# Optimization experiments

Measured on AMD Instinct MI355X. Metric: run time of the kernel, lower is better.

## Reference

```python
import jax, jax.numpy as jnp
import numpy as np
from jax import lax

B, F, N = 1024, 512, 8  # batch, feature_dim, num_of_subAttention


def setup_inputs() -> dict:
    key = jax.random.key(0)
    ks = jax.random.split(key, 8)
    sc = 0.02
    return {
        "vx": jax.random.normal(ks[0], (B, F), dtype=jnp.float32),
        "ax": jax.random.normal(ks[1], (B, F), dtype=jnp.float32),
        # stacked per-unit MLP params (N units)
        "W1": jax.random.normal(ks[2], (N, F, 2 * F), dtype=jnp.float32) * sc,
        "b1": jnp.zeros((N, F), jnp.float32),
        "W2": jax.random.normal(ks[3], (N, F, F), dtype=jnp.float32) * sc,
        "b2": jnp.zeros((N, F), jnp.float32),
        # conv pipeline params (OIHW)
        "conv1_w": jax.random.normal(ks[4], (F, F, 3, 3), dtype=jnp.float32) * sc,
        "conv1_b": jnp.zeros((F,), jnp.float32),
        "conv2_w": jax.random.normal(ks[5], (F, F, 3, 3), dtype=jnp.float32) * sc,
        "conv2_b": jnp.zeros((F,), jnp.float32),
    }


def reference(vx, ax, W1, b1, W2, b2, conv1_w, conv1_b, conv2_w, conv2_b):
    # --- N AttentionUnits, vectorized over the unit axis n ---
    x = jnp.concatenate([vx, ax], axis=-1)                      # [B, 2F]
    # Dropout(0.5) is identity in eval mode.
    h = jax.nn.relu(jnp.einsum('bi,nfi->bnf', x, W1) + b1)      # [B, N, F]
    att = jax.nn.relu(jnp.einsum('bnf,ngf->bng', h, W2) + b2)   # [B, N, F]

    # vx broadcast over units, elementwise attention, then permute to [B, F, N]
    va = jnp.transpose(vx[:, None, :] * att, (0, 2, 1))         # [B, F, N]
    # rank-1 broadcast along trailing axis -> conv input [B, F, N, N]
    t = jnp.broadcast_to(va[..., None], (B, F, N, N))

    dn = ('NCHW', 'OIHW', 'NCHW')
    y = lax.conv_general_dilated(t, conv1_w, (1, 1), 'SAME', dimension_numbers=dn)
    y = y + conv1_b[None, :, None, None]
    k = N // 2
    y = lax.reduce_window(y, -jnp.inf, lax.max, (1, 1, k, k), (1, 1, k, k), 'VALID')  # [B,F,2,2]
    y = lax.conv_general_dilated(y, conv2_w, (1, 1), 'SAME', dimension_numbers=dn)
    y = y + conv2_b[None, :, None, None]
    y = jnp.mean(y, axis=(2, 3))                                # AdaptiveAvgPool2d((1,1)) -> [B, F]
    return jax.nn.relu(y)
```

## Files before the change

kernel.cpp:

```cpp
#include <hip/hip_runtime.h>
#include <hip/hip_bf16.h>


typedef __attribute__((ext_vector_type(8))) short short8;
typedef __attribute__((ext_vector_type(4))) float f32x4;

__device__ __forceinline__ void gload16(const void* g, void* l) {
    __builtin_amdgcn_global_load_lds(
        (const __attribute__((address_space(1))) void*)g,
        (__attribute__((address_space(3))) void*)l, 16, 0, 0);
}

template<int BM, int BN, bool RELU, bool BIAS, bool OUT_BF16, bool SWAP>
__global__ __launch_bounds__(256) void gemm_mfma(
    const __hip_bfloat16* __restrict__ A, int lda, long sA,
    const __hip_bfloat16* __restrict__ B, int ldb, long sB,
    void* __restrict__ Cv, int ldc, long sC,
    const float* __restrict__ bias, long sBias,
    int K)
{
    constexpr int MI = BM / 32, NI = BN / 32;
    constexpr int GA = BM / 16, GB = BN / 16;
    constexpr int nA = (GA * 2) / 4, nB = (GB * 2) / 4;
    __shared__ __align__(16) char As[128 * BM];
    __shared__ __align__(16) char Bs[128 * BN];

    const int z = blockIdx.z;
    A += (long)z * sA;
    B += (long)z * sB;
    const int bm = (SWAP ? blockIdx.x : blockIdx.y) * BM;
    const int bn = (SWAP ? blockIdx.y : blockIdx.x) * BN;
    const int t = threadIdx.x, lane = t & 63, wid = t >> 6;
    const int q = lane >> 4, lr = lane & 15;
    const int wrow = (wid >> 1) * (BM / 2), wcol = (wid & 1) * (BN / 2);

    const int m_loc = lane >> 2;
    const int cst = ((lane & 3) - (m_loc >> 1)) & 3;
    const long abase = ((long)(bm + m_loc) * lda + cst * 8) * 2;
    const long bbase = ((long)(bn + m_loc) * ldb + cst * 8) * 2;

    const int ro = lr * 4;

    f32x4 acc[MI][NI] = {};

    for (int k0 = 0; k0 < K; k0 += 64) {
        if (k0) __syncthreads();
        #pragma unroll
        for (int i = 0; i < nA; ++i) {
            int s = wid * nA + i, g = s % GA, h = s / GA;
            const char* gp = (const char*)A + abase + ((long)g * 16 * lda + h * 32 + k0) * 2;
            gload16(gp, As + (h * (BM * 4) + g * 64) * 16);
        }
        #pragma unroll
        for (int i = 0; i < nB; ++i) {
            int s = wid * nB + i, g = s % GB, h = s / GB;
            const char* gp = (const char*)B + bbase + ((long)g * 16 * ldb + h * 32 + k0) * 2;
            gload16(gp, Bs + (h * (BN * 4) + g * 64) * 16);
        }
        __syncthreads();

        #pragma unroll
        for (int ks = 0; ks < 2; ++ks) {
            short8 af[MI], bf[NI];
            #pragma unroll
            for (int mi = 0; mi < MI; ++mi) {
                int u = ks * (BM * 4) + ((wrow >> 4) + mi) * 64 + ro + ((q + (lr >> 1)) & 3);
                af[mi] = *(const short8*)(As + u * 16);
            }
            #pragma unroll
            for (int ni = 0; ni < NI; ++ni) {
                int u = ks * (BN * 4) + ((wcol >> 4) + ni) * 64 + ro + ((q + (lr >> 1)) & 3);
                bf[ni] = *(const short8*)(Bs + u * 16);
            }
            #pragma unroll
            for (int mi = 0; mi < MI; ++mi)
                #pragma unroll
                for (int ni = 0; ni < NI; ++ni)
                    acc[mi][ni] = __builtin_amdgcn_mfma_f32_16x16x32_bf16(
                        af[mi], bf[ni], acc[mi][ni], 0, 0, 0);
        }
    }

    #pragma unroll
    for (int mi = 0; mi < MI; ++mi) {
        #pragma unroll
        for (int ni = 0; ni < NI; ++ni) {
            int gn = bn + wcol + ni * 16 + lr;
            float bv = 0.f;
            if constexpr (BIAS) bv = bias[z * sBias + gn];
            #pragma unroll
            for (int r = 0; r < 4; ++r) {
                long gm = bm + wrow + mi * 16 + q * 4 + r;
                float v = acc[mi][ni][r] + bv;
                if constexpr (RELU) v = fmaxf(v, 0.f);
                if constexpr (OUT_BF16)
                    ((__hip_bfloat16*)Cv)[z * sC + gm * ldc + gn] = __float2bfloat16(v);
                else
                    ((float*)Cv)[z * sC + gm * ldc + gn] = v;
            }
        }
    }
}

__global__ void concat_kernel(const float* __restrict__ vx,
                              const float* __restrict__ ax,
                              __hip_bfloat16* __restrict__ x)
{
    int i = blockIdx.x * 256 + threadIdx.x;
    int b = i >> 9, c = i & 511;
    x[((long)b << 10) + c]       = __float2bfloat16(vx[i]);
    x[((long)b << 10) + 512 + c] = __float2bfloat16(ax[i]);
}

__global__ void cast2_kernel(const float* __restrict__ w1,
                             __hip_bfloat16* __restrict__ o1,
                             const float* __restrict__ w2,
                             __hip_bfloat16* __restrict__ o2)
{
    int i = blockIdx.x * 256 + threadIdx.x;
    const float* src = (i < 1048576) ? w1 : w2;
    __hip_bfloat16* dst = (i < 1048576) ? o1 : o2;
    int j = (i < 1048576) ? i : i - 1048576;
    float4 v = ((const float4*)src)[j];
    union { __hip_bfloat16 h[4]; short4 s; } u;
    u.h[0] = __float2bfloat16(v.x); u.h[1] = __float2bfloat16(v.y);
    u.h[2] = __float2bfloat16(v.z); u.h[3] = __float2bfloat16(v.w);
    ((short4*)dst)[j] = u.s;
}

__global__ void im2col_kernel(const float* __restrict__ vx,
                              const __hip_bfloat16* __restrict__ att,
                              __hip_bfloat16* __restrict__ A1)
{
    int col = blockIdx.x * 256 + threadIdx.x;
    int row = blockIdx.y;
    int b = row >> 3, i = row & 7;
    int ki = col >> 9, c = col & 511;
    int ip = i + ki - 1;
    float v = 0.f;
    if (ip >= 0 && ip < 8)
        v = vx[(b << 9) + c] * __bfloat162float(att[((long)b << 12) + (ip << 9) + c]);
    A1[(long)row * 1536 + col] = __float2bfloat16(v);
}

__global__ void wcat_kernel(const float* __restrict__ w1c,
                            __hip_bfloat16* __restrict__ Wcat)
{
    int col = blockIdx.x * 256 + threadIdx.x;
    int row = blockIdx.y;
    int v = row >> 9, o = row & 511;
    int ki = col >> 9, c = col & 511;
    const float* w = w1c + ((long)(o * 512 + c) * 3 + ki) * 3;
    float s = w[1];
    if (v != 0) s += w[0];
    if (v != 2) s += w[2];
    Wcat[(long)row * 1536 + col] = __float2bfloat16(s);
}

__global__ void pool_kernel(const __hip_bfloat16* __restrict__ Y1,
                            const float* __restrict__ c1b,
                            __hip_bfloat16* __restrict__ P)
{
    int idx = blockIdx.x * 256 + threadIdx.x;
    int b = idx >> 9, o = idx & 511;
    const __hip_bfloat16* y = Y1 + (long)b * 8 * 1536 + o;
    float bias = c1b[o];
    float pv[2][2];
    #pragma unroll
    for (int pi = 0; pi < 2; ++pi) {
        float m0 = -3.402823466e38f, m1 = -3.402823466e38f;
        #pragma unroll
        for (int r = 0; r < 4; ++r) {
            int i = pi * 4 + r;
            float yl = __bfloat162float(y[i * 1536 + 0]);
            float ym = __bfloat162float(y[i * 1536 + 512]);
            float yr = __bfloat162float(y[i * 1536 + 1024]);
            m0 = fmaxf(m0, fmaxf(yl, ym));
            m1 = fmaxf(m1, fmaxf(ym, yr));
        }
        pv[pi][0] = m0; pv[pi][1] = m1;
    }
    __hip_bfloat16* pp = P + ((long)b * 2048) + o * 4;
    pp[0] = __float2bfloat16(pv[0][0] + bias);
    pp[1] = __float2bfloat16(pv[0][1] + bias);
    pp[2] = __float2bfloat16(pv[1][0] + bias);
    pp[3] = __float2bfloat16(pv[1][1] + bias);
}

__global__ void m2_kernel(const float* __restrict__ w2c,
                          __hip_bfloat16* __restrict__ M2)
{
    int col = blockIdx.x * 256 + threadIdx.x;
    int o2  = blockIdx.y;
    int c = col >> 2, pi = (col >> 1) & 1, pj = col & 1;
    const float* w = w2c + (long)(o2 * 512 + c) * 9;
    float s = w[pi * 3 + pj] + w[pi * 3 + pj + 1]
            + w[(pi + 1) * 3 + pj] + w[(pi + 1) * 3 + pj + 1];
    M2[(long)o2 * 2048 + col] = __float2bfloat16(0.25f * s);
}

extern "C" void kernel_launch(void* const* d_in, const int* in_sizes, int n_in,
                              void* d_out, int out_size, void* d_ws, size_t ws_size,
                              hipStream_t stream)
{
    const float* vx  = (const float*)d_in[0];
    const float* ax  = (const float*)d_in[1];
    const float* W1  = (const float*)d_in[2];
    const float* b1  = (const float*)d_in[3];
    const float* W2  = (const float*)d_in[4];
    const float* b2  = (const float*)d_in[5];
    const float* c1w = (const float*)d_in[6];
    const float* c1b = (const float*)d_in[7];
    const float* c2w = (const float*)d_in[8];
    const float* c2b = (const float*)d_in[9];
    float* out = (float*)d_out;
    char* w = (char*)d_ws;

    const long MiB = 1 << 20;
    __hip_bfloat16* Xbf   = (__hip_bfloat16*)(w + 0 * MiB);
    __hip_bfloat16* W1bf  = (__hip_bfloat16*)(w + 2 * MiB);
    __hip_bfloat16* Hbf   = (__hip_bfloat16*)(w + 10 * MiB);
    __hip_bfloat16* W2bf  = (__hip_bfloat16*)(w + 18 * MiB);
    __hip_bfloat16* ATTbf = (__hip_bfloat16*)(w + 22 * MiB);
    __hip_bfloat16* A1bf  = (__hip_bfloat16*)(w + 30 * MiB);
    __hip_bfloat16* WCbf  = (__hip_bfloat16*)(w + 54 * MiB);
    __hip_bfloat16* Y1bf  = (__hip_bfloat16*)(w + 59 * MiB);
    __hip_bfloat16* Pbf   = (__hip_bfloat16*)(w + 83 * MiB);
    __hip_bfloat16* M2bf  = (__hip_bfloat16*)(w + 87 * MiB);

    concat_kernel<<<2048, 256, 0, stream>>>(vx, ax, Xbf);
    cast2_kernel<<<6144, 256, 0, stream>>>(W1, W1bf, W2, W2bf);

    gemm_mfma<128, 128, true, true, true, false><<<dim3(32, 8, 1), 256, 0, stream>>>(
        Xbf, 1024, 0, W1bf, 1024, 0, Hbf, 4096, 0, b1, 0, 1024);

    gemm_mfma<128, 128, true, true, true, false><<<dim3(4, 8, 8), 256, 0, stream>>>(
        Hbf, 4096, 512, W2bf, 512, 262144, ATTbf, 4096, 512, b2, 512, 512);

    im2col_kernel<<<dim3(6, 8192), 256, 0, stream>>>(vx, ATTbf, A1bf);
    wcat_kernel<<<dim3(6, 1536), 256, 0, stream>>>(c1w, WCbf);

    gemm_mfma<128, 128, false, false, true, true><<<dim3(64, 12, 1), 256, 0, stream>>>(
        A1bf, 1536, 0, WCbf, 1536, 0, Y1bf, 1536, 0, nullptr, 0, 1536);

    pool_kernel<<<2048, 256, 0, stream>>>(Y1bf, c1b, Pbf);
    m2_kernel<<<dim3(8, 512), 256, 0, stream>>>(c2w, M2bf);

    gemm_mfma<64, 64, true, true, false, false><<<dim3(8, 16, 1), 256, 0, stream>>>(
        Pbf, 2048, 0, M2bf, 2048, 0, out, 512, 0, c2b, 0, 2048);
}
```

Before: 233.1 us.

## Fuse conv GEMM with partial max-pool epilogue and merge prep kernels

Merges the four weight and input preparation kernels into one launch. The conv1 GEMM now max-reduces each group of 4 accumulator rows in its epilogue and writes fp32 partial pooled values, so the full bf16 Y1 intermediate no longer has to be written and read back. A small combine kernel then takes the max across the three column views, adds the bias, and writes the packed bf16 input for the final GEMM. This cuts launches and global-memory traffic, at the cost of a larger, divergent prep kernel and an extra fp32 intermediate buffer.

Result: faster. 223.7 us (-4.0%).

```diff
diff --git a/kernel.cpp b/kernel.cpp
--- a/kernel.cpp
+++ b/kernel.cpp
@@ -38,8 +38,8 @@
     const int cst = ((lane & 3) - (m_loc >> 1)) & 3;
     const long abase = ((long)(bm + m_loc) * lda + cst * 8) * 2;
     const long bbase = ((long)(bn + m_loc) * ldb + cst * 8) * 2;
-
     const int ro = lr * 4;
+    const int csel = (lr >> 1);
 
     f32x4 acc[MI][NI] = {};
 
@@ -48,14 +48,14 @@
         #pragma unroll
         for (int i = 0; i < nA; ++i) {
             int s = wid * nA + i, g = s % GA, h = s / GA;
-            const char* gp = (const char*)A + abase + ((long)g * 16 * lda + h * 32 + k0) * 2;
-            gload16(gp, As + (h * (BM * 4) + g * 64) * 16);
+            gload16((const char*)A + abase + ((long)g * 16 * lda + h * 32 + k0) * 2,
+                    As + (h * (BM * 4) + g * 64) * 16);
         }
         #pragma unroll
         for (int i = 0; i < nB; ++i) {
             int s = wid * nB + i, g = s % GB, h = s / GB;
-            const char* gp = (const char*)B + bbase + ((long)g * 16 * ldb + h * 32 + k0) * 2;
-            gload16(gp, Bs + (h * (BN * 4) + g * 64) * 16);
+            gload16((const char*)B + bbase + ((long)g * 16 * ldb + h * 32 + k0) * 2,
+                    Bs + (h * (BN * 4) + g * 64) * 16);
         }
         __syncthreads();
 
@@ -64,12 +64,12 @@
             short8 af[MI], bf[NI];
             #pragma unroll
             for (int mi = 0; mi < MI; ++mi) {
-                int u = ks * (BM * 4) + ((wrow >> 4) + mi) * 64 + ro + ((q + (lr >> 1)) & 3);
+                int u = ks * (BM * 4) + ((wrow >> 4) + mi) * 64 + ro + ((q + csel) & 3);
                 af[mi] = *(const short8*)(As + u * 16);
             }
             #pragma unroll
             for (int ni = 0; ni < NI; ++ni) {
-                int u = ks * (BN * 4) + ((wcol >> 4) + ni) * 64 + ro + ((q + (lr >> 1)) & 3);
+                int u = ks * (BN * 4) + ((wcol >> 4) + ni) * 64 + ro + ((q + csel) & 3);
                 bf[ni] = *(const short8*)(Bs + u * 16);
             }
             #pragma unroll
@@ -102,30 +102,84 @@
     }
 }
 
-__global__ void concat_kernel(const float* __restrict__ vx,
-                              const float* __restrict__ ax,
-                              __hip_bfloat16* __restrict__ x)
-{
-    int i = blockIdx.x * 256 + threadIdx.x;
-    int b = i >> 9, c = i & 511;
-    x[((long)b << 10) + c]       = __float2bfloat16(vx[i]);
-    x[((long)b << 10) + 512 + c] = __float2bfloat16(ax[i]);
-}
-
-__global__ void cast2_kernel(const float* __restrict__ w1,
-                             __hip_bfloat16* __restrict__ o1,
-                             const float* __restrict__ w2,
-                             __hip_bfloat16* __restrict__ o2)
-{
-    int i = blockIdx.x * 256 + threadIdx.x;
-    const float* src = (i < 1048576) ? w1 : w2;
-    __hip_bfloat16* dst = (i < 1048576) ? o1 : o2;
-    int j = (i < 1048576) ? i : i - 1048576;
-    float4 v = ((const float4*)src)[j];
-    union { __hip_bfloat16 h[4]; short4 s; } u;
-    u.h[0] = __float2bfloat16(v.x); u.h[1] = __float2bfloat16(v.y);
-    u.h[2] = __float2bfloat16(v.z); u.h[3] = __float2bfloat16(v.w);
-    ((short4*)dst)[j] = u.s;
+__global__ __launch_bounds__(256) void conv_gemm_pool(
+    const __hip_bfloat16* __restrict__ A,
+    const __hip_bfloat16* __restrict__ B,
+    float* __restrict__ PM)
+{
+    constexpr int BM = 128, BN = 128, MI = 4, NI = 4;
+    constexpr int GA = 8, GB = 8, nA = 4, nB = 4;
+    const int lda = 1536, ldb = 1536, K = 1536;
+    __shared__ __align__(16) char As[128 * BM];
+    __shared__ __align__(16) char Bs[128 * BN];
+
+    const int bm = blockIdx.x * BM;
+    const int bn = blockIdx.y * BN;
+    const int t = threadIdx.x, lane = t & 63, wid = t >> 6;
+    const int q = lane >> 4, lr = lane & 15;
+    const int wrow = (wid >> 1) * 64, wcol = (wid & 1) * 64;
+
+    const int m_loc = lane >> 2;
+    const int cst = ((lane & 3) - (m_loc >> 1)) & 3;
+    const long abase = ((long)(bm + m_loc) * lda + cst * 8) * 2;
+    const long bbase = ((long)(bn + m_loc) * ldb + cst * 8) * 2;
+    const int ro = lr * 4;
+    const int csel = (lr >> 1);
+
+    f32x4 acc[MI][NI] = {};
+
+    for (int k0 = 0; k0 < K; k0 += 64) {
+        if (k0) __syncthreads();
+        #pragma unroll
+        for (int i = 0; i < nA; ++i) {
+            int s = wid * nA + i, g = s % GA, h = s / GA;
+            gload16((const char*)A + abase + ((long)g * 16 * lda + h * 32 + k0) * 2,
+                    As + (h * (BM * 4) + g * 64) * 16);
+        }
+        #pragma unroll
+        for (int i = 0; i < nB; ++i) {
+            int s = wid * nB + i, g = s % GB, h = s / GB;
+            gload16((const char*)B + bbase + ((long)g * 16 * ldb + h * 32 + k0) * 2,
+                    Bs + (h * (BN * 4) + g * 64) * 16);
+        }
+        __syncthreads();
+
+        #pragma unroll
+        for (int ks = 0; ks < 2; ++ks) {
+            short8 af[MI], bf[NI];
+            #pragma unroll
+            for (int mi = 0; mi < MI; ++mi) {
+                int u = ks * (BM * 4) + ((wrow >> 4) + mi) * 64 + ro + ((q + csel) & 3);
+                af[mi] = *(const short8*)(As + u * 16);
+            }
+            #pragma unroll
+            for (int ni = 0; ni < NI; ++ni) {
+                int u = ks * (BN * 4) + ((wcol >> 4) + ni) * 64 + ro + ((q + csel) & 3);
+                bf[ni] = *(const short8*)(Bs + u * 16);
+            }
+            #pragma unroll
+            for (int mi = 0; mi < MI; ++mi)
+                #pragma unroll
+                for (int ni = 0; ni < NI; ++ni)
+                    acc[mi][ni] = __builtin_amdgcn_mfma_f32_16x16x32_bf16(
+                        af[mi], bf[ni], acc[mi][ni], 0, 0, 0);
+        }
+    }
+
+    #pragma unroll
+    for (int mi = 0; mi < MI; ++mi) {
+        int rowbase = bm + wrow + mi * 16;
+        int batch = (rowbase >> 3) + (q >> 1);
+        int pi = q & 1;
+        #pragma unroll
+        for (int ni = 0; ni < NI; ++ni) {
+            int gn = bn + wcol + ni * 16 + lr;
+            int v = gn >> 9, o = gn & 511;
+            float m = fmaxf(fmaxf(acc[mi][ni][0], acc[mi][ni][1]),
+                            fmaxf(acc[mi][ni][2], acc[mi][ni][3]));
+            PM[((long)v * 1024 + batch) * 1024 + pi * 512 + o] = m;
+        }
+    }
 }
 
 __global__ void im2col_kernel(const float* __restrict__ vx,
@@ -143,60 +197,68 @@
     A1[(long)row * 1536 + col] = __float2bfloat16(v);
 }
 
-__global__ void wcat_kernel(const float* __restrict__ w1c,
-                            __hip_bfloat16* __restrict__ Wcat)
-{
-    int col = blockIdx.x * 256 + threadIdx.x;
-    int row = blockIdx.y;
-    int v = row >> 9, o = row & 511;
-    int ki = col >> 9, c = col & 511;
-    const float* w = w1c + ((long)(o * 512 + c) * 3 + ki) * 3;
-    float s = w[1];
-    if (v != 0) s += w[0];
-    if (v != 2) s += w[2];
-    Wcat[(long)row * 1536 + col] = __float2bfloat16(s);
-}
-
-__global__ void pool_kernel(const __hip_bfloat16* __restrict__ Y1,
-                            const float* __restrict__ c1b,
-                            __hip_bfloat16* __restrict__ P)
+__global__ __launch_bounds__(256) void prep_kernel(
+    const float* __restrict__ vx, const float* __restrict__ ax,
+    const float* __restrict__ W1, const float* __restrict__ W2,
+    const float* __restrict__ c1w, const float* __restrict__ c2w,
+    __hip_bfloat16* __restrict__ X,  __hip_bfloat16* __restrict__ W1b,
+    __hip_bfloat16* __restrict__ W2b, __hip_bfloat16* __restrict__ WC,
+    __hip_bfloat16* __restrict__ M2)
+{
+    int blk = blockIdx.x, t = threadIdx.x;
+    if (blk < 2048) {
+        int i = blk * 256 + t, b = i >> 9, c = i & 511;
+        X[((long)b << 10) + c]       = __float2bfloat16(vx[i]);
+        X[((long)b << 10) + 512 + c] = __float2bfloat16(ax[i]);
+    } else if (blk < 8192) {
+        int j = (blk - 2048) * 256 + t;
+        const float* src = (j < 1048576) ? W1 : W2;
+        __hip_bfloat16* dst = (j < 1048576) ? W1b : W2b;
+        int k = (j < 1048576) ? j : j - 1048576;
+        float4 v = ((const float4*)src)[k];
+        union { __hip_bfloat16 h[4]; short4 s; } u;
+        u.h[0] = __float2bfloat16(v.x); u.h[1] = __float2bfloat16(v.y);
+        u.h[2] = __float2bfloat16(v.z); u.h[3] = __float2bfloat16(v.w);
+        ((short4*)dst)[k] = u.s;
+    } else if (blk < 17408) {
+        int b2 = blk - 8192;
+        int row = b2 / 6, col = (b2 % 6) * 256 + t;
+        int v = row >> 9, o = row & 511;
+        int ki = col >> 9, c = col & 511;
+        const float* w = c1w + ((long)(o * 512 + c) * 3 + ki) * 3;
+        float s = w[1];
+        if (v != 0) s += w[0];
+        if (v != 2) s += w[2];
+        WC[(long)row * 1536 + col] = __float2bfloat16(s);
+    } else {
+        int b2 = blk - 17408;
+        int o2 = b2 >> 3, col = (b2 & 7) * 256 + t;
+        int c = col >> 2, pi = (col >> 1) & 1, pj = col & 1;
+        const float* w = c2w + (long)(o2 * 512 + c) * 9;
+        float s = w[pi * 3 + pj] + w[pi * 3 + pj + 1]
+                + w[(pi + 1) * 3 + pj] + w[(pi + 1) * 3 + pj + 1];
+        M2[(long)o2 * 2048 + col] = __float2bfloat16(0.25f * s);
+    }
+}
+
+__global__ __launch_bounds__(256) void combine_kernel(
+    const float* __restrict__ PM, const float* __restrict__ c1b,
+    __hip_bfloat16* __restrict__ P)
 {
     int idx = blockIdx.x * 256 + threadIdx.x;
     int b = idx >> 9, o = idx & 511;
-    const __hip_bfloat16* y = Y1 + (long)b * 8 * 1536 + o;
     float bias = c1b[o];
-    float pv[2][2];
-    #pragma unroll
-    for (int pi = 0; pi < 2; ++pi) {
-        float m0 = -3.402823466e38f, m1 = -3.402823466e38f;
-        #pragma unroll
-        for (int r = 0; r < 4; ++r) {
-            int i = pi * 4 + r;
-            float yl = __bfloat162float(y[i * 1536 + 0]);
-            float ym = __bfloat162float(y[i * 1536 + 512]);
-            float yr = __bfloat162float(y[i * 1536 + 1024]);
-            m0 = fmaxf(m0, fmaxf(yl, ym));
-            m1 = fmaxf(m1, fmaxf(ym, yr));
-        }
-        pv[pi][0] = m0; pv[pi][1] = m1;
-    }
-    __hip_bfloat16* pp = P + ((long)b * 2048) + o * 4;
-    pp[0] = __float2bfloat16(pv[0][0] + bias);
-    pp[1] = __float2bfloat16(pv[0][1] + bias);
-    pp[2] = __float2bfloat16(pv[1][0] + bias);
-    pp[3] = __float2bfloat16(pv[1][1] + bias);
-}
-
-__global__ void m2_kernel(const float* __restrict__ w2c,
-                          __hip_bfloat16* __restrict__ M2)
-{
-    int col = blockIdx.x * 256 + threadIdx.x;
-    int o2  = blockIdx.y;
-    int c = col >> 2, pi = (col >> 1) & 1, pj = col & 1;
-    const float* w = w2c + (long)(o2 * 512 + c) * 9;
-    float s = w[pi * 3 + pj] + w[pi * 3 + pj + 1]
-            + w[(pi + 1) * 3 + pj] + w[(pi + 1) * 3 + pj + 1];
-    M2[(long)o2 * 2048 + col] = __float2bfloat16(0.25f * s);
+    const long vs = 1024L * 1024;
+    long base = (long)b * 1024 + o;
+    float l0 = PM[base],            l1 = PM[base + 512];
+    float m0 = PM[vs + base],       m1 = PM[vs + base + 512];
+    float r0 = PM[2 * vs + base],   r1 = PM[2 * vs + base + 512];
+    union { __hip_bfloat16 h[4]; short4 s; } u;
+    u.h[0] = __float2bfloat16(fmaxf(l0, m0) + bias);
+    u.h[1] = __float2bfloat16(fmaxf(m0, r0) + bias);
+    u.h[2] = __float2bfloat16(fmaxf(l1, m1) + bias);
+    u.h[3] = __float2bfloat16(fmaxf(m1, r1) + bias);
+    ((short4*)(P + (long)b * 2048 + o * 4))[0] = u.s;
 }
 
 extern "C" void kernel_launch(void* const* d_in, const int* in_sizes, int n_in,
@@ -224,12 +286,12 @@
     __hip_bfloat16* ATTbf = (__hip_bfloat16*)(w + 22 * MiB);
     __hip_bfloat16* A1bf  = (__hip_bfloat16*)(w + 30 * MiB);
     __hip_bfloat16* WCbf  = (__hip_bfloat16*)(w + 54 * MiB);
-    __hip_bfloat16* Y1bf  = (__hip_bfloat16*)(w + 59 * MiB);
-    __hip_bfloat16* Pbf   = (__hip_bfloat16*)(w + 83 * MiB);
-    __hip_bfloat16* M2bf  = (__hip_bfloat16*)(w + 87 * MiB);
-
-    concat_kernel<<<2048, 256, 0, stream>>>(vx, ax, Xbf);
-    cast2_kernel<<<6144, 256, 0, stream>>>(W1, W1bf, W2, W2bf);
+    float*          PM    = (float*)         (w + 59 * MiB);
+    __hip_bfloat16* Pbf   = (__hip_bfloat16*)(w + 71 * MiB);
+    __hip_bfloat16* M2bf  = (__hip_bfloat16*)(w + 75 * MiB);
+
+    prep_kernel<<<21504, 256, 0, stream>>>(vx, ax, W1, W2, c1w, c2w,
+                                           Xbf, W1bf, W2bf, WCbf, M2bf);
 
     gemm_mfma<128, 128, true, true, true, false><<<dim3(32, 8, 1), 256, 0, stream>>>(
         Xbf, 1024, 0, W1bf, 1024, 0, Hbf, 4096, 0, b1, 0, 1024);
@@ -238,13 +300,10 @@
         Hbf, 4096, 512, W2bf, 512, 262144, ATTbf, 4096, 512, b2, 512, 512);
 
     im2col_kernel<<<dim3(6, 8192), 256, 0, stream>>>(vx, ATTbf, A1bf);
-    wcat_kernel<<<dim3(6, 1536), 256, 0, stream>>>(c1w, WCbf);
-
-    gemm_mfma<128, 128, false, false, true, true><<<dim3(64, 12, 1), 256, 0, stream>>>(
-        A1bf, 1536, 0, WCbf, 1536, 0, Y1bf, 1536, 0, nullptr, 0, 1536);
-
-    pool_kernel<<<2048, 256, 0, stream>>>(Y1bf, c1b, Pbf);
-    m2_kernel<<<dim3(8, 512), 256, 0, stream>>>(c2w, M2bf);
+
+    conv_gemm_pool<<<dim3(64, 12), 256, 0, stream>>>(A1bf, WCbf, PM);
+
+    combine_kernel<<<2048, 256, 0, stream>>>(PM, c1b, Pbf);
 
     gemm_mfma<64, 64, true, true, false, false><<<dim3(8, 16, 1), 256, 0, stream>>>(
         Pbf, 2048, 0, M2bf, 2048, 0, out, 512, 0, c2b, 0, 2048);
```
